# Kernel tuning notes

Measured on AMD Instinct MI355X. Metric: run time of the kernel, lower is better.

Reference implementation:

```python
import jax, jax.numpy as jnp
import numpy as np

B, N, D, P, K = 4, 2048, 512, 16, 4
EPS_BW = 1e-8
EPS_LN = 1e-5


def setup_inputs() -> dict:
    key = jax.random.key(0)
    ks = jax.random.split(key, 8)
    charge = jax.random.normal(ks[0], (B, N, D), dtype=jnp.float32)
    position = jax.random.normal(ks[1], (B, N, P), dtype=jnp.float32)
    mass = jax.random.uniform(ks[2], (B, N, 1), dtype=jnp.float32)
    # parameters
    log_bandwidth = jnp.zeros((K,), dtype=jnp.float32)
    W_charge = jax.random.normal(ks[3], (D * K, D), dtype=jnp.float32) / np.sqrt(D)   # torch Linear weight (out,in)
    W_combine = jax.random.normal(ks[4], (D, D * K), dtype=jnp.float32) / np.sqrt(D * K)
    gamma = jnp.ones((D,), dtype=jnp.float32)
    beta = jnp.zeros((D,), dtype=jnp.float32)
    return {"charge": charge, "position": position, "mass": mass,
            "log_bandwidth": log_bandwidth, "W_charge": W_charge,
            "W_combine": W_combine, "gamma": gamma, "beta": beta}


def reference(charge, position, mass, log_bandwidth, W_charge, W_combine, gamma, beta):
    # pairwise squared distances: (B, N, N)
    diff = position[:, :, None, :] - position[:, None, :, :]
    dist_sq = jnp.sum(diff * diff, axis=-1)
    # multi-bandwidth Gaussian kernels: (B, N, N, K)
    bandwidths = jnp.exp(log_bandwidth)
    kernels = jnp.exp(-dist_sq[..., None] / (2.0 * bandwidths + EPS_BW))
    # mass weighting: mass (B,N,1) -> (B,1,N,1), broadcast over query axis and kernels
    weighted_kernels = kernels * mass[:, None, :, :]
    # project charges: (B, N, K, D)
    projected = (charge @ W_charge.T).reshape(B, N, K, D)
    # aggregate over neighbours j: field[b,i,k,d] = sum_j wk[b,i,j,k] * proj[b,j,k,d]
    field = jnp.einsum('bijk,bjkd->bikd', weighted_kernels, projected)
    field = field.reshape(B, N, K * D) @ W_combine.T  # (B, N, D)
    # LayerNorm
    mean = jnp.mean(field, axis=-1, keepdims=True)
    var = jnp.var(field, axis=-1, keepdims=True)
    normed = (field - mean) * jax.lax.rsqrt(var + EPS_LN)
    return normed * gamma + beta
```

## Files before the change

kernel.cpp:

```cpp
#include <hip/hip_runtime.h>


typedef __bf16 bf16x8 __attribute__((ext_vector_type(8)));
typedef float f32x4 __attribute__((ext_vector_type(4)));

__device__ __forceinline__ unsigned short f2bf(float f) {
    unsigned u = __float_as_uint(f);
    unsigned r = (u + 0x7fffu + ((u >> 16) & 1u)) >> 16;
    return (unsigned short)r;
}
__device__ __forceinline__ float bf2f(unsigned short h) {
    return __uint_as_float(((unsigned)h) << 16);
}
__device__ __forceinline__ void g2l16(const unsigned short* g, unsigned short* l) {
    __builtin_amdgcn_global_load_lds(
        (const __attribute__((address_space(1))) unsigned int*)g,
        (__attribute__((address_space(3))) unsigned int*)l, 16, 0, 0);
}

__global__ __launch_bounds__(256) void k0_pos(const float* __restrict__ pos,
                                              unsigned short* __restrict__ posA,
                                              unsigned short* __restrict__ posB1,
                                              unsigned short* __restrict__ posB2,
                                              float* __restrict__ rsq)
{
    const int row = blockIdx.x * 256 + threadIdx.x;
    const float* src = &pos[(size_t)row * 16];
    float p[16];
#pragma unroll
    for (int cc = 0; cc < 4; cc++) {
        float4 v = *reinterpret_cast<const float4*>(&src[cc * 4]);
        p[cc * 4 + 0] = v.x; p[cc * 4 + 1] = v.y; p[cc * 4 + 2] = v.z; p[cc * 4 + 3] = v.w;
    }
    float r = 0.f;
    unsigned short h[16], lo[16], z[8] = {0, 0, 0, 0, 0, 0, 0, 0};
#pragma unroll
    for (int d = 0; d < 16; d++) {
        r = __builtin_fmaf(p[d], p[d], r);
        h[d] = f2bf(p[d]);
        lo[d] = f2bf(p[d] - bf2f(h[d]));
    }
    rsq[row] = r;
    size_t o = (size_t)row * 32;
    *reinterpret_cast<int4*>(&posA[o + 0])   = *reinterpret_cast<int4*>(&h[0]);
    *reinterpret_cast<int4*>(&posA[o + 8])   = *reinterpret_cast<int4*>(&h[8]);
    *reinterpret_cast<int4*>(&posA[o + 16])  = *reinterpret_cast<int4*>(&lo[0]);
    *reinterpret_cast<int4*>(&posA[o + 24])  = *reinterpret_cast<int4*>(&lo[8]);
    *reinterpret_cast<int4*>(&posB1[o + 0])  = *reinterpret_cast<int4*>(&h[0]);
    *reinterpret_cast<int4*>(&posB1[o + 8])  = *reinterpret_cast<int4*>(&h[8]);
    *reinterpret_cast<int4*>(&posB1[o + 16]) = *reinterpret_cast<int4*>(&h[0]);
    *reinterpret_cast<int4*>(&posB1[o + 24]) = *reinterpret_cast<int4*>(&h[8]);
    *reinterpret_cast<int4*>(&posB2[o + 0])  = *reinterpret_cast<int4*>(&lo[0]);
    *reinterpret_cast<int4*>(&posB2[o + 8])  = *reinterpret_cast<int4*>(&lo[8]);
    *reinterpret_cast<int4*>(&posB2[o + 16]) = *reinterpret_cast<int4*>(&z[0]);
    *reinterpret_cast<int4*>(&posB2[o + 24]) = *reinterpret_cast<int4*>(&z[0]);
}

__global__ __launch_bounds__(256) void k0_cvt(const float* __restrict__ src,
                                              unsigned short* __restrict__ dst)
{
    size_t i = (size_t)blockIdx.x * 256 + threadIdx.x;
    float4 v = reinterpret_cast<const float4*>(src)[i];
    unsigned short o[4] = {f2bf(v.x), f2bf(v.y), f2bf(v.z), f2bf(v.w)};
    reinterpret_cast<uint2*>(dst)[i] = *reinterpret_cast<uint2*>(&o[0]);
}

__global__ __launch_bounds__(256, 2) void k1_proj(const unsigned short* __restrict__ wc16,
                                                  const unsigned short* __restrict__ ch16,
                                                  const float* __restrict__ mass,
                                                  unsigned short* __restrict__ projm_t)
{
    __shared__ alignas(16) unsigned short As[128 * 32];
    __shared__ alignas(16) unsigned short Bs[128 * 32];
    const int tid = threadIdx.x, lane = tid & 63, wid = tid >> 6;
    const int q = lane >> 4, l15 = lane & 15;
    const int sw = (l15 >> 2) & 3;
    const int m0 = blockIdx.y * 128, n0 = blockIdx.x * 128;
    const int wm = (wid & 1) * 64, wn = (wid >> 1) * 64;

    f32x4 acc[4][4];
#pragma unroll
    for (int i = 0; i < 4; i++)
#pragma unroll
        for (int j = 0; j < 4; j++) acc[i][j] = (f32x4){0.f, 0.f, 0.f, 0.f};

    for (int k0 = 0; k0 < 512; k0 += 32) {
        __syncthreads();
#pragma unroll
        for (int q4 = 0; q4 < 4; q4++) {
            int chunk = q4 * 256 + tid;
            int w = chunk & 511, row = w >> 2;
            int gc4 = (w & 3) ^ ((w >> 4) & 3);
            if (chunk < 512)
                g2l16(&wc16[(size_t)(m0 + row) * 512 + k0 + gc4 * 8], &As[w * 8]);
            else
                g2l16(&ch16[(size_t)(n0 + row) * 512 + k0 + gc4 * 8], &Bs[w * 8]);
        }
        __syncthreads();
        bf16x8 af[4], bfr[4];
#pragma unroll
        for (int it = 0; it < 4; it++)
            af[it] = *reinterpret_cast<const bf16x8*>(&As[(wm + it * 16 + l15) * 32 + (q ^ sw) * 8]);
#pragma unroll
        for (int ct = 0; ct < 4; ct++)
            bfr[ct] = *reinterpret_cast<const bf16x8*>(&Bs[(wn + ct * 16 + l15) * 32 + (q ^ sw) * 8]);
#pragma unroll
        for (int it = 0; it < 4; it++)
#pragma unroll
            for (int ct = 0; ct < 4; ct++)
                acc[it][ct] = __builtin_amdgcn_mfma_f32_16x16x32_bf16(af[it], bfr[ct], acc[it][ct], 0, 0, 0);
    }
#pragma unroll
    for (int ct = 0; ct < 4; ct++) {
        int n = n0 + wn + ct * 16 + l15;
        float mf = mass[n];
#pragma unroll
        for (int it = 0; it < 4; it++) {
            int mrow = m0 + wm + it * 16 + q * 4;
#pragma unroll
            for (int r = 0; r < 4; r++)
                projm_t[(size_t)(mrow + r) * 8192 + n] = f2bf(acc[it][ct][r] * mf);
        }
    }
}

__global__ __launch_bounds__(256, 2) void k2_field(const unsigned short* __restrict__ posA,
                                                   const unsigned short* __restrict__ posB1,
                                                   const unsigned short* __restrict__ posB2,
                                                   const float* __restrict__ rsq,
                                                   const float* __restrict__ logbw,
                                                   const unsigned short* __restrict__ projm_t,
                                                   unsigned short* __restrict__ field)
{
    __shared__ alignas(16) unsigned short Bs[2][256 * 32];
    __shared__ alignas(16) unsigned short Wl[2][128 * 40];

    const int tid = threadIdx.x, lane = tid & 63, wid = tid >> 6;
    const int q = lane >> 4, l15 = lane & 15;
    const int sw = (l15 >> 2) & 3;
    const int L = blockIdx.x;
    const int xcd = L & 7, idx = L >> 3;
    const int i_t = idx & 15, cb = xcd * 4 + (idx >> 4);
    const int c0 = (cb & 7) * 256, b = cb >> 3;
    const int i0 = i_t * 128;
    const int kb = c0 >> 9;
    const float bw = __expf(logbw[kb]);
    const float s2 = -1.4426950408889634f / (2.0f * bw + 1e-8f);
    const float c2 = -2.0f * s2;
    const int bN = b * 2048;

    bf16x8 afG[2];
    float riS2[2][4];
#pragma unroll
    for (int t = 0; t < 2; t++) {
        afG[t] = *reinterpret_cast<const bf16x8*>(
            &posA[(size_t)(bN + i0 + wid * 32 + t * 16 + l15) * 32 + q * 8]);
#pragma unroll
        for (int r = 0; r < 4; r++)
            riS2[t][r] = rsq[bN + i0 + wid * 32 + t * 16 + q * 4 + r] * s2;
    }

    const int wo_i = (wid >> 1) * 64, wo_c = (wid & 1) * 128;

    f32x4 acc[4][8];
#pragma unroll
    for (int i = 0; i < 4; i++)
#pragma unroll
        for (int j = 0; j < 8; j++) acc[i][j] = (f32x4){0.f, 0.f, 0.f, 0.f};

    for (int j0 = 0; j0 < 2048; j0 += 64) {
        unsigned short wv[2][2][2][4];
#pragma unroll
        for (int s = 0; s < 2; s++) {
#pragma unroll
            for (int jt2 = 0; jt2 < 2; jt2++) {
                int j = bN + j0 + s * 32 + jt2 * 16 + l15;
                bf16x8 b1 = *reinterpret_cast<const bf16x8*>(&posB1[(size_t)j * 32 + q * 8]);
                bf16x8 b2 = *reinterpret_cast<const bf16x8*>(&posB2[(size_t)j * 32 + q * 8]);
                float rj2 = rsq[j] * s2;
#pragma unroll
                for (int t = 0; t < 2; t++) {
                    f32x4 g = (f32x4){0.f, 0.f, 0.f, 0.f};
                    g = __builtin_amdgcn_mfma_f32_16x16x32_bf16(afG[t], b2, g, 0, 0, 0);
                    g = __builtin_amdgcn_mfma_f32_16x16x32_bf16(afG[t], b1, g, 0, 0, 0);
#pragma unroll
                    for (int r = 0; r < 4; r++) {
                        float x = __builtin_fmaf(g[r], c2, riS2[t][r] + rj2);
                        wv[s][jt2][t][r] = f2bf(__builtin_amdgcn_exp2f(x));
                    }
                }
            }
        }
        __syncthreads();
#pragma unroll
        for (int s = 0; s < 2; s++)
#pragma unroll
            for (int jt2 = 0; jt2 < 2; jt2++)
#pragma unroll
                for (int t = 0; t < 2; t++)
#pragma unroll
                    for (int r = 0; r < 4; r++)
                        Wl[s][(wid * 32 + t * 16 + q * 4 + r) * 40 + jt2 * 16 + l15] =
                            wv[s][jt2][t][r];
        {
            const size_t gb = (size_t)c0 * 8192 + bN + j0;
#pragma unroll
            for (int q8 = 0; q8 < 8; q8++) {
                int chunk = q8 * 256 + tid;
                int s = chunk >> 10, w1 = chunk & 1023;
                int row = w1 >> 2, gc4 = (w1 & 3) ^ ((w1 >> 4) & 3);
                g2l16(&projm_t[gb + (size_t)row * 8192 + s * 32 + gc4 * 8], &Bs[s][w1 * 8]);
            }
        }
        __syncthreads();
#pragma unroll
        for (int s = 0; s < 2; s++) {
            bf16x8 af[4], bfr[8];
#pragma unroll
            for (int it = 0; it < 4; it++)
                af[it] = *reinterpret_cast<const bf16x8*>(&Wl[s][(wo_i + it * 16 + l15) * 40 + q * 8]);
#pragma unroll
            for (int ct = 0; ct < 8; ct++)
                bfr[ct] = *reinterpret_cast<const bf16x8*>(&Bs[s][(wo_c + ct * 16 + l15) * 32 + (q ^ sw) * 8]);
#pragma unroll
            for (int it = 0; it < 4; it++)
#pragma unroll
                for (int ct = 0; ct < 8; ct++)
                    acc[it][ct] = __builtin_amdgcn_mfma_f32_16x16x32_bf16(af[it], bfr[ct], acc[it][ct], 0, 0, 0);
        }
    }
#pragma unroll
    for (int it = 0; it < 4; it++) {
#pragma unroll
        for (int ct = 0; ct < 8; ct++) {
            int gi = bN + i0 + wo_i + it * 16 + q * 4;
            int gc = c0 + wo_c + ct * 16 + l15;
#pragma unroll
            for (int r = 0; r < 4; r++)
                field[(size_t)(gi + r) * 2048 + gc] = f2bf(acc[it][ct][r]);
        }
    }
}

__global__ __launch_bounds__(256, 2) void k3_combine(const unsigned short* __restrict__ field,
                                                     const unsigned short* __restrict__ wcb16,
                                                     float* __restrict__ out)
{
    __shared__ alignas(16) unsigned short As[64 * 32];
    __shared__ alignas(16) unsigned short Bs[128 * 32];
    const int tid = threadIdx.x, lane = tid & 63, wid = tid >> 6;
    const int q = lane >> 4, l15 = lane & 15;
    const int sw = (l15 >> 2) & 3;
    const int m0 = blockIdx.y * 64, n0 = blockIdx.x * 128;
    const int wn = wid * 32;

    f32x4 acc[4][2];
#pragma unroll
    for (int i = 0; i < 4; i++)
#pragma unroll
        for (int j = 0; j < 2; j++) acc[i][j] = (f32x4){0.f, 0.f, 0.f, 0.f};

    for (int k0 = 0; k0 < 2048; k0 += 32) {
        __syncthreads();
#pragma unroll
        for (int q3 = 0; q3 < 3; q3++) {
            int chunk = q3 * 256 + tid;
            if (chunk < 256) {
                int row = chunk >> 2, gc4 = (chunk & 3) ^ ((chunk >> 4) & 3);
                g2l16(&field[(size_t)(m0 + row) * 2048 + k0 + gc4 * 8], &As[chunk * 8]);
            } else {
                int w = chunk - 256, row = w >> 2, gc4 = (w & 3) ^ ((w >> 4) & 3);
                g2l16(&wcb16[(size_t)(n0 + row) * 2048 + k0 + gc4 * 8], &Bs[w * 8]);
            }
        }
        __syncthreads();
        bf16x8 af[4], bfr[2];
#pragma unroll
        for (int it = 0; it < 4; it++)
            af[it] = *reinterpret_cast<const bf16x8*>(&As[(it * 16 + l15) * 32 + (q ^ sw) * 8]);
#pragma unroll
        for (int ct = 0; ct < 2; ct++)
            bfr[ct] = *reinterpret_cast<const bf16x8*>(&Bs[(wn + ct * 16 + l15) * 32 + (q ^ sw) * 8]);
#pragma unroll
        for (int it = 0; it < 4; it++)
#pragma unroll
            for (int ct = 0; ct < 2; ct++)
                acc[it][ct] = __builtin_amdgcn_mfma_f32_16x16x32_bf16(af[it], bfr[ct], acc[it][ct], 0, 0, 0);
    }
#pragma unroll
    for (int it = 0; it < 4; it++) {
#pragma unroll
        for (int ct = 0; ct < 2; ct++) {
            int m = m0 + it * 16 + q * 4;
            int n = n0 + wn + ct * 16 + l15;
#pragma unroll
            for (int r = 0; r < 4; r++)
                out[(size_t)(m + r) * 512 + n] = acc[it][ct][r];
        }
    }
}

__global__ __launch_bounds__(256) void k4_ln(float* __restrict__ out,
                                             const float* __restrict__ gamma,
                                             const float* __restrict__ beta)
{
    __shared__ float red[8];
    const int row = blockIdx.x, tid = threadIdx.x;
    float2 x = *reinterpret_cast<const float2*>(&out[(size_t)row * 512 + tid * 2]);
    float s = x.x + x.y;
    float ss = x.x * x.x + x.y * x.y;
#pragma unroll
    for (int off = 32; off > 0; off >>= 1) {
        s += __shfl_down(s, off);
        ss += __shfl_down(ss, off);
    }
    int wid = tid >> 6;
    if ((tid & 63) == 0) { red[wid * 2] = s; red[wid * 2 + 1] = ss; }
    __syncthreads();
    s = red[0] + red[2] + red[4] + red[6];
    ss = red[1] + red[3] + red[5] + red[7];
    float mean = s * (1.f / 512.f);
    float var = ss * (1.f / 512.f) - mean * mean;
    float inv = rsqrtf(var + 1e-5f);
    float g0 = gamma[tid * 2], g1 = gamma[tid * 2 + 1];
    float b0 = beta[tid * 2], b1 = beta[tid * 2 + 1];
    float2 o;
    o.x = (x.x - mean) * inv * g0 + b0;
    o.y = (x.y - mean) * inv * g1 + b1;
    *reinterpret_cast<float2*>(&out[(size_t)row * 512 + tid * 2]) = o;
}

extern "C" void kernel_launch(void* const* d_in, const int* in_sizes, int n_in,
                              void* d_out, int out_size, void* d_ws, size_t ws_size,
                              hipStream_t stream)
{
    const float* charge   = (const float*)d_in[0];
    const float* position = (const float*)d_in[1];
    const float* mass     = (const float*)d_in[2];
    const float* logbw    = (const float*)d_in[3];
    const float* Wc       = (const float*)d_in[4];
    const float* Wcb      = (const float*)d_in[5];
    const float* gamma    = (const float*)d_in[6];
    const float* beta     = (const float*)d_in[7];

    unsigned short* projm_t = (unsigned short*)d_ws;
    unsigned short* field   = projm_t + (size_t)2048 * 8192;
    unsigned short* wcb16   = projm_t;
    unsigned short* ch16    = field;
    unsigned short* wc16    = field + (size_t)8192 * 512;
    unsigned short* posA  = (unsigned short*)d_out;
    unsigned short* posB1 = posA + (size_t)8192 * 32;
    unsigned short* posB2 = posB1 + (size_t)8192 * 32;
    float* rsq = (float*)(posB2 + (size_t)8192 * 32);
    float* out = (float*)d_out;

    k0_pos<<<32, 256, 0, stream>>>(position, posA, posB1, posB2, rsq);
    k0_cvt<<<4096, 256, 0, stream>>>(charge, ch16);
    k0_cvt<<<1024, 256, 0, stream>>>(Wc, wc16);
    k1_proj<<<dim3(64, 16), 256, 0, stream>>>(wc16, ch16, mass, projm_t);
    k2_field<<<512, 256, 0, stream>>>(posA, posB1, posB2, rsq, logbw, projm_t, field);
    k0_cvt<<<1024, 256, 0, stream>>>(Wcb, wcb16);
    k3_combine<<<dim3(4, 128), 256, 0, stream>>>(field, wcb16, out);
    k4_ln<<<8192, 256, 0, stream>>>(out, gamma, beta);
}
```

Before: 260.8 us.

## Pipeline LDS tile loads in GEMM kernels and fuse preprocessing launches

The three preprocessing kernels (charge and W_charge bf16 conversion, position split) are merged into one launch. The projection and combine GEMMs gain double-buffered LDS, so the next K-tile is prefetched while MFMAs run on the current one, with one barrier per step; their occupancy hint rises to 3. The field kernel is restructured to 32-column steps: the Gaussian weights go straight into ping-pong LDS buffers, and projm tiles are prefetched through a triple buffer. This trades more LDS per block and finer-grained steps for overlap of global loads with compute and fewer barriers per tile.

```diff
diff --git a/kernel.cpp b/kernel.cpp
--- a/kernel.cpp
+++ b/kernel.cpp
@@ -18,13 +18,27 @@
         (__attribute__((address_space(3))) unsigned int*)l, 16, 0, 0);
 }
 
-__global__ __launch_bounds__(256) void k0_pos(const float* __restrict__ pos,
+__global__ __launch_bounds__(256) void k0_all(const float* __restrict__ charge,
+                                              const float* __restrict__ Wc,
+                                              const float* __restrict__ pos,
+                                              unsigned short* __restrict__ ch16,
+                                              unsigned short* __restrict__ wc16,
                                               unsigned short* __restrict__ posA,
                                               unsigned short* __restrict__ posB1,
                                               unsigned short* __restrict__ posB2,
                                               float* __restrict__ rsq)
 {
-    const int row = blockIdx.x * 256 + threadIdx.x;
+    const int bx = blockIdx.x, tid = threadIdx.x;
+    if (bx < 5120) {
+        const float* src = (bx < 4096) ? charge : Wc;
+        unsigned short* dst = (bx < 4096) ? ch16 : wc16;
+        size_t i = (size_t)(bx < 4096 ? bx : bx - 4096) * 256 + tid;
+        float4 v = reinterpret_cast<const float4*>(src)[i];
+        unsigned short o[4] = {f2bf(v.x), f2bf(v.y), f2bf(v.z), f2bf(v.w)};
+        reinterpret_cast<uint2*>(dst)[i] = *reinterpret_cast<uint2*>(&o[0]);
+        return;
+    }
+    const int row = (bx - 5120) * 256 + tid;
     const float* src = &pos[(size_t)row * 16];
     float p[16];
 #pragma unroll
@@ -65,13 +79,13 @@
     reinterpret_cast<uint2*>(dst)[i] = *reinterpret_cast<uint2*>(&o[0]);
 }
 
-__global__ __launch_bounds__(256, 2) void k1_proj(const unsigned short* __restrict__ wc16,
+__global__ __launch_bounds__(256, 3) void k1_proj(const unsigned short* __restrict__ wc16,
                                                   const unsigned short* __restrict__ ch16,
                                                   const float* __restrict__ mass,
                                                   unsigned short* __restrict__ projm_t)
 {
-    __shared__ alignas(16) unsigned short As[128 * 32];
-    __shared__ alignas(16) unsigned short Bs[128 * 32];
+    __shared__ alignas(16) unsigned short As[2][128 * 32];
+    __shared__ alignas(16) unsigned short Bs[2][128 * 32];
     const int tid = threadIdx.x, lane = tid & 63, wid = tid >> 6;
     const int q = lane >> 4, l15 = lane & 15;
     const int sw = (l15 >> 2) & 3;
@@ -84,42 +98,60 @@
 #pragma unroll
         for (int j = 0; j < 4; j++) acc[i][j] = (f32x4){0.f, 0.f, 0.f, 0.f};
 
-    for (int k0 = 0; k0 < 512; k0 += 32) {
-        __syncthreads();
-#pragma unroll
-        for (int q4 = 0; q4 < 4; q4++) {
-            int chunk = q4 * 256 + tid;
-            int w = chunk & 511, row = w >> 2;
-            int gc4 = (w & 3) ^ ((w >> 4) & 3);
-            if (chunk < 512)
-                g2l16(&wc16[(size_t)(m0 + row) * 512 + k0 + gc4 * 8], &As[w * 8]);
-            else
-                g2l16(&ch16[(size_t)(n0 + row) * 512 + k0 + gc4 * 8], &Bs[w * 8]);
-        }
-        __syncthreads();
+    const int w = tid & 255;
+    (void)w;
+
+#pragma unroll
+    for (int q4 = 0; q4 < 4; q4++) {
+        int chunk = q4 * 256 + tid;
+        int ww = chunk & 511, row = ww >> 2;
+        int gc4 = (ww & 3) ^ ((ww >> 4) & 3);
+        if (chunk < 512)
+            g2l16(&wc16[(size_t)(m0 + row) * 512 + gc4 * 8], &As[0][ww * 8]);
+        else
+            g2l16(&ch16[(size_t)(n0 + row) * 512 + gc4 * 8], &Bs[0][ww * 8]);
+    }
+    __syncthreads();
+
+    for (int n = 0; n < 16; n++) {
+        const int p = n & 1;
+        const int k1 = (n + 1) * 32;
+        if (k1 < 512) {
+#pragma unroll
+            for (int q4 = 0; q4 < 4; q4++) {
+                int chunk = q4 * 256 + tid;
+                int ww = chunk & 511, row = ww >> 2;
+                int gc4 = (ww & 3) ^ ((ww >> 4) & 3);
+                if (chunk < 512)
+                    g2l16(&wc16[(size_t)(m0 + row) * 512 + k1 + gc4 * 8], &As[p ^ 1][ww * 8]);
+                else
+                    g2l16(&ch16[(size_t)(n0 + row) * 512 + k1 + gc4 * 8], &Bs[p ^ 1][ww * 8]);
+            }
+        }
         bf16x8 af[4], bfr[4];
 #pragma unroll
         for (int it = 0; it < 4; it++)
-            af[it] = *reinterpret_cast<const bf16x8*>(&As[(wm + it * 16 + l15) * 32 + (q ^ sw) * 8]);
+            af[it] = *reinterpret_cast<const bf16x8*>(&As[p][(wm + it * 16 + l15) * 32 + (q ^ sw) * 8]);
 #pragma unroll
         for (int ct = 0; ct < 4; ct++)
-            bfr[ct] = *reinterpret_cast<const bf16x8*>(&Bs[(wn + ct * 16 + l15) * 32 + (q ^ sw) * 8]);
+            bfr[ct] = *reinterpret_cast<const bf16x8*>(&Bs[p][(wn + ct * 16 + l15) * 32 + (q ^ sw) * 8]);
 #pragma unroll
         for (int it = 0; it < 4; it++)
 #pragma unroll
             for (int ct = 0; ct < 4; ct++)
                 acc[it][ct] = __builtin_amdgcn_mfma_f32_16x16x32_bf16(af[it], bfr[ct], acc[it][ct], 0, 0, 0);
+        __syncthreads();
     }
 #pragma unroll
     for (int ct = 0; ct < 4; ct++) {
-        int n = n0 + wn + ct * 16 + l15;
-        float mf = mass[n];
+        int nn = n0 + wn + ct * 16 + l15;
+        float mf = mass[nn];
 #pragma unroll
         for (int it = 0; it < 4; it++) {
             int mrow = m0 + wm + it * 16 + q * 4;
 #pragma unroll
             for (int r = 0; r < 4; r++)
-                projm_t[(size_t)(mrow + r) * 8192 + n] = f2bf(acc[it][ct][r] * mf);
+                projm_t[(size_t)(mrow + r) * 8192 + nn] = f2bf(acc[it][ct][r] * mf);
         }
     }
 }
@@ -132,7 +164,7 @@
                                                    const unsigned short* __restrict__ projm_t,
                                                    unsigned short* __restrict__ field)
 {
-    __shared__ alignas(16) unsigned short Bs[2][256 * 32];
+    __shared__ alignas(16) unsigned short Bs[3][256 * 32];
     __shared__ alignas(16) unsigned short Wl[2][128 * 40];
 
     const int tid = threadIdx.x, lane = tid & 63, wid = tid >> 6;
@@ -161,6 +193,7 @@
     }
 
     const int wo_i = (wid >> 1) * 64, wo_c = (wid & 1) * 128;
+    const size_t gbase = (size_t)c0 * 8192 + bN;
 
     f32x4 acc[4][8];
 #pragma unroll
@@ -168,66 +201,65 @@
 #pragma unroll
         for (int j = 0; j < 8; j++) acc[i][j] = (f32x4){0.f, 0.f, 0.f, 0.f};
 
-    for (int j0 = 0; j0 < 2048; j0 += 64) {
-        unsigned short wv[2][2][2][4];
-#pragma unroll
-        for (int s = 0; s < 2; s++) {
-#pragma unroll
-            for (int jt2 = 0; jt2 < 2; jt2++) {
-                int j = bN + j0 + s * 32 + jt2 * 16 + l15;
-                bf16x8 b1 = *reinterpret_cast<const bf16x8*>(&posB1[(size_t)j * 32 + q * 8]);
-                bf16x8 b2 = *reinterpret_cast<const bf16x8*>(&posB2[(size_t)j * 32 + q * 8]);
-                float rj2 = rsq[j] * s2;
-#pragma unroll
-                for (int t = 0; t < 2; t++) {
-                    f32x4 g = (f32x4){0.f, 0.f, 0.f, 0.f};
-                    g = __builtin_amdgcn_mfma_f32_16x16x32_bf16(afG[t], b2, g, 0, 0, 0);
-                    g = __builtin_amdgcn_mfma_f32_16x16x32_bf16(afG[t], b1, g, 0, 0, 0);
-#pragma unroll
-                    for (int r = 0; r < 4; r++) {
-                        float x = __builtin_fmaf(g[r], c2, riS2[t][r] + rj2);
-                        wv[s][jt2][t][r] = f2bf(__builtin_amdgcn_exp2f(x));
-                    }
+#pragma unroll
+    for (int q4 = 0; q4 < 4; q4++) {
+        int chunk = q4 * 256 + tid;
+        int row = chunk >> 2, gc4 = (chunk & 3) ^ ((chunk >> 4) & 3);
+        g2l16(&projm_t[gbase + (size_t)row * 8192 + gc4 * 8], &Bs[0][chunk * 8]);
+    }
+
+    int bs_r = 0;
+    for (int n = 0; n < 64; n++) {
+        const int j0 = n * 32;
+        const int p = n & 1;
+        bf16x8 gb1[2], gb2[2];
+        float rj2[2];
+#pragma unroll
+        for (int jt2 = 0; jt2 < 2; jt2++) {
+            int j = bN + j0 + jt2 * 16 + l15;
+            gb1[jt2] = *reinterpret_cast<const bf16x8*>(&posB1[(size_t)j * 32 + q * 8]);
+            gb2[jt2] = *reinterpret_cast<const bf16x8*>(&posB2[(size_t)j * 32 + q * 8]);
+            rj2[jt2] = rsq[j] * s2;
+        }
+        if (j0 + 32 < 2048) {
+            const int bs_w = bs_r + 1 == 3 ? 0 : bs_r + 1;
+            const size_t gb = gbase + j0 + 32;
+#pragma unroll
+            for (int q4 = 0; q4 < 4; q4++) {
+                int chunk = q4 * 256 + tid;
+                int row = chunk >> 2, gc4 = (chunk & 3) ^ ((chunk >> 4) & 3);
+                g2l16(&projm_t[gb + (size_t)row * 8192 + gc4 * 8], &Bs[bs_w][chunk * 8]);
+            }
+        }
+#pragma unroll
+        for (int jt2 = 0; jt2 < 2; jt2++) {
+#pragma unroll
+            for (int t = 0; t < 2; t++) {
+                f32x4 g = (f32x4){0.f, 0.f, 0.f, 0.f};
+                g = __builtin_amdgcn_mfma_f32_16x16x32_bf16(afG[t], gb2[jt2], g, 0, 0, 0);
+                g = __builtin_amdgcn_mfma_f32_16x16x32_bf16(afG[t], gb1[jt2], g, 0, 0, 0);
+#pragma unroll
+                for (int r = 0; r < 4; r++) {
+                    float x = __builtin_fmaf(g[r], c2, riS2[t][r] + rj2[jt2]);
+                    Wl[p][(wid * 32 + t * 16 + q * 4 + r) * 40 + jt2 * 16 + l15] =
+                        f2bf(__builtin_amdgcn_exp2f(x));
                 }
             }
         }
         __syncthreads();
-#pragma unroll
-        for (int s = 0; s < 2; s++)
-#pragma unroll
-            for (int jt2 = 0; jt2 < 2; jt2++)
-#pragma unroll
-                for (int t = 0; t < 2; t++)
-#pragma unroll
-                    for (int r = 0; r < 4; r++)
-                        Wl[s][(wid * 32 + t * 16 + q * 4 + r) * 40 + jt2 * 16 + l15] =
-                            wv[s][jt2][t][r];
-        {
-            const size_t gb = (size_t)c0 * 8192 + bN + j0;
-#pragma unroll
-            for (int q8 = 0; q8 < 8; q8++) {
-                int chunk = q8 * 256 + tid;
-                int s = chunk >> 10, w1 = chunk & 1023;
-                int row = w1 >> 2, gc4 = (w1 & 3) ^ ((w1 >> 4) & 3);
-                g2l16(&projm_t[gb + (size_t)row * 8192 + s * 32 + gc4 * 8], &Bs[s][w1 * 8]);
-            }
-        }
-        __syncthreads();
-#pragma unroll
-        for (int s = 0; s < 2; s++) {
-            bf16x8 af[4], bfr[8];
-#pragma unroll
-            for (int it = 0; it < 4; it++)
-                af[it] = *reinterpret_cast<const bf16x8*>(&Wl[s][(wo_i + it * 16 + l15) * 40 + q * 8]);
+        bf16x8 af[4], bfr[8];
+#pragma unroll
+        for (int it = 0; it < 4; it++)
+            af[it] = *reinterpret_cast<const bf16x8*>(&Wl[p][(wo_i + it * 16 + l15) * 40 + q * 8]);
+#pragma unroll
+        for (int ct = 0; ct < 8; ct++)
+            bfr[ct] = *reinterpret_cast<const bf16x8*>(&Bs[bs_r][(wo_c + ct * 16 + l15) * 32 + (q ^ sw) * 8]);
+#pragma unroll
+        for (int it = 0; it < 4; it++)
 #pragma unroll
             for (int ct = 0; ct < 8; ct++)
-                bfr[ct] = *reinterpret_cast<const bf16x8*>(&Bs[s][(wo_c + ct * 16 + l15) * 32 + (q ^ sw) * 8]);
-#pragma unroll
-            for (int it = 0; it < 4; it++)
-#pragma unroll
-                for (int ct = 0; ct < 8; ct++)
-                    acc[it][ct] = __builtin_amdgcn_mfma_f32_16x16x32_bf16(af[it], bfr[ct], acc[it][ct], 0, 0, 0);
-        }
+                acc[it][ct] = __builtin_amdgcn_mfma_f32_16x16x32_bf16(af[it], bfr[ct], acc[it][ct], 0, 0, 0);
+        bs_r = bs_r + 1 == 3 ? 0 : bs_r + 1;
     }
 #pragma unroll
     for (int it = 0; it < 4; it++) {
@@ -242,12 +274,12 @@
     }
 }
 
-__global__ __launch_bounds__(256, 2) void k3_combine(const unsigned short* __restrict__ field,
+__global__ __launch_bounds__(256, 3) void k3_combine(const unsigned short* __restrict__ field,
                                                      const unsigned short* __restrict__ wcb16,
                                                      float* __restrict__ out)
 {
-    __shared__ alignas(16) unsigned short As[64 * 32];
-    __shared__ alignas(16) unsigned short Bs[128 * 32];
+    __shared__ alignas(16) unsigned short As[2][64 * 32];
+    __shared__ alignas(16) unsigned short Bs[2][128 * 32];
     const int tid = threadIdx.x, lane = tid & 63, wid = tid >> 6;
     const int q = lane >> 4, l15 = lane & 15;
     const int sw = (l15 >> 2) & 3;
@@ -260,42 +292,58 @@
 #pragma unroll
         for (int j = 0; j < 2; j++) acc[i][j] = (f32x4){0.f, 0.f, 0.f, 0.f};
 
-    for (int k0 = 0; k0 < 2048; k0 += 32) {
-        __syncthreads();
-#pragma unroll
-        for (int q3 = 0; q3 < 3; q3++) {
-            int chunk = q3 * 256 + tid;
-            if (chunk < 256) {
-                int row = chunk >> 2, gc4 = (chunk & 3) ^ ((chunk >> 4) & 3);
-                g2l16(&field[(size_t)(m0 + row) * 2048 + k0 + gc4 * 8], &As[chunk * 8]);
-            } else {
-                int w = chunk - 256, row = w >> 2, gc4 = (w & 3) ^ ((w >> 4) & 3);
-                g2l16(&wcb16[(size_t)(n0 + row) * 2048 + k0 + gc4 * 8], &Bs[w * 8]);
+#pragma unroll
+    for (int q3 = 0; q3 < 3; q3++) {
+        int chunk = q3 * 256 + tid;
+        if (chunk < 256) {
+            int row = chunk >> 2, gc4 = (chunk & 3) ^ ((chunk >> 4) & 3);
+            g2l16(&field[(size_t)(m0 + row) * 2048 + gc4 * 8], &As[0][chunk * 8]);
+        } else {
+            int ww = chunk - 256, row = ww >> 2, gc4 = (ww & 3) ^ ((ww >> 4) & 3);
+            g2l16(&wcb16[(size_t)(n0 + row) * 2048 + gc4 * 8], &Bs[0][ww * 8]);
+        }
+    }
+    __syncthreads();
+
+    for (int n = 0; n < 64; n++) {
+        const int p = n & 1;
+        const int k1 = (n + 1) * 32;
+        if (k1 < 2048) {
+#pragma unroll
+            for (int q3 = 0; q3 < 3; q3++) {
+                int chunk = q3 * 256 + tid;
+                if (chunk < 256) {
+                    int row = chunk >> 2, gc4 = (chunk & 3) ^ ((chunk >> 4) & 3);
+                    g2l16(&field[(size_t)(m0 + row) * 2048 + k1 + gc4 * 8], &As[p ^ 1][chunk * 8]);
+                } else {
+                    int ww = chunk - 256, row = ww >> 2, gc4 = (ww & 3) ^ ((ww >> 4) & 3);
+                    g2l16(&wcb16[(size_t)(n0 + row) * 2048 + k1 + gc4 * 8], &Bs[p ^ 1][ww * 8]);
+                }
             }
         }
-        __syncthreads();
         bf16x8 af[4], bfr[2];
 #pragma unroll
         for (int it = 0; it < 4; it++)
-            af[it] = *reinterpret_cast<const bf16x8*>(&As[(it * 16 + l15) * 32 + (q ^ sw) * 8]);
+            af[it] = *reinterpret_cast<const bf16x8*>(&As[p][(it * 16 + l15) * 32 + (q ^ sw) * 8]);
 #pragma unroll
         for (int ct = 0; ct < 2; ct++)
-            bfr[ct] = *reinterpret_cast<const bf16x8*>(&Bs[(wn + ct * 16 + l15) * 32 + (q ^ sw) * 8]);
+            bfr[ct] = *reinterpret_cast<const bf16x8*>(&Bs[p][(wn + ct * 16 + l15) * 32 + (q ^ sw) * 8]);
 #pragma unroll
         for (int it = 0; it < 4; it++)
 #pragma unroll
             for (int ct = 0; ct < 2; ct++)
                 acc[it][ct] = __builtin_amdgcn_mfma_f32_16x16x32_bf16(af[it], bfr[ct], acc[it][ct], 0, 0, 0);
+        __syncthreads();
     }
 #pragma unroll
     for (int it = 0; it < 4; it++) {
 #pragma unroll
         for (int ct = 0; ct < 2; ct++) {
             int m = m0 + it * 16 + q * 4;
-            int n = n0 + wn + ct * 16 + l15;
+            int nn = n0 + wn + ct * 16 + l15;
 #pragma unroll
             for (int r = 0; r < 4; r++)
-                out[(size_t)(m + r) * 512 + n] = acc[it][ct][r];
+                out[(size_t)(m + r) * 512 + nn] = acc[it][ct][r];
         }
     }
 }
@@ -354,9 +402,7 @@
     float* rsq = (float*)(posB2 + (size_t)8192 * 32);
     float* out = (float*)d_out;
 
-    k0_pos<<<32, 256, 0, stream>>>(position, posA, posB1, posB2, rsq);
-    k0_cvt<<<4096, 256, 0, stream>>>(charge, ch16);
-    k0_cvt<<<1024, 256, 0, stream>>>(Wc, wc16);
+    k0_all<<<5152, 256, 0, stream>>>(charge, Wc, position, ch16, wc16, posA, posB1, posB2, rsq);
     k1_proj<<<dim3(64, 16), 256, 0, stream>>>(wc16, ch16, mass, projm_t);
     k2_field<<<512, 256, 0, stream>>>(posA, posB1, posB2, rsq, logbw, projm_t, field);
     k0_cvt<<<1024, 256, 0, stream>>>(Wcb, wcb16);
```

Result: no change. 263.1 us (+0.9%).
